# Kernel tuning notes

Measured on AMD Instinct MI355X. Metric: run time of the kernel, lower is better.

Reference implementation:

```python
import jax, jax.numpy as jnp
import numpy as np

B, H, F, E, K = 32, 4096, 4096, 8, 2

def setup_inputs() -> dict:
    key = jax.random.key(0)
    ks = jax.random.split(key, 5)
    x = jax.random.normal(ks[0], (B, H), dtype=jnp.float32)
    Wg = jax.random.normal(ks[1], (H, E), dtype=jnp.float32) * 0.02
    W1 = jax.random.normal(ks[2], (E, H, F), dtype=jnp.float32) * 0.02
    W3 = jax.random.normal(ks[3], (E, H, F), dtype=jnp.float32) * 0.02
    W2 = jax.random.normal(ks[4], (E, F, H), dtype=jnp.float32) * 0.02
    return {"x": x, "Wg": Wg, "W1": W1, "W3": W3, "W2": W2}

def reference(x, Wg, W1, W3, W2):
    # Gate: [B, E] logits, top-2 selection, softmax over the 2 selected logits
    logits = x @ Wg                                   # [B, E]
    vals, idx = jax.lax.top_k(logits, K)              # [B, K]
    w = jax.nn.softmax(vals, axis=-1)                 # [B, K]
    # Combine weights per expert: [B, E] (zero for unselected experts)
    combine = jnp.sum(jax.nn.one_hot(idx, E, dtype=x.dtype) * w[..., None], axis=1)
    h = jnp.einsum('bh,ehf->ebf', x, W1)              # [E, B, F]
    g = jax.nn.silu(h) * jnp.einsum('bh,ehf->ebf', x, W3)
    y = jnp.einsum('ebf,efh->ebh', g, W2)             # [E, B, H]
    # Scatter-combine: weighted sum over experts (all-gather + reduce-sum in source)
    return jnp.einsum('be,ebh->bh', combine, y)       # [B, H]
```

## Files before the change

kernel.cpp:

```cpp
#include <hip/hip_runtime.h>
#include <cstdint>

#define BB 32
#define HH 4096
#define FF 4096
#define EE 8
#define NSLOT 16
#define TSEG 16

__global__ __launch_bounds__(256) void gate_kernel(const float* __restrict__ x,
                                                   const float* __restrict__ Wg,
                                                   float* __restrict__ logits) {
  int b = blockIdx.x;
  int tid = threadIdx.x;
  float acc[EE];
#pragma unroll
  for (int e = 0; e < EE; ++e) acc[e] = 0.f;
  const float* xb = x + (size_t)b * HH;
  for (int h = tid; h < HH; h += 256) {
    float xv = xb[h];
    const float4* wg = (const float4*)(Wg + (size_t)h * EE);
    float4 w0 = wg[0], w1 = wg[1];
    acc[0] = fmaf(xv, w0.x, acc[0]);
    acc[1] = fmaf(xv, w0.y, acc[1]);
    acc[2] = fmaf(xv, w0.z, acc[2]);
    acc[3] = fmaf(xv, w0.w, acc[3]);
    acc[4] = fmaf(xv, w1.x, acc[4]);
    acc[5] = fmaf(xv, w1.y, acc[5]);
    acc[6] = fmaf(xv, w1.z, acc[6]);
    acc[7] = fmaf(xv, w1.w, acc[7]);
  }
#pragma unroll
  for (int off = 32; off > 0; off >>= 1) {
#pragma unroll
    for (int e = 0; e < EE; ++e) acc[e] += __shfl_down(acc[e], off, 64);
  }
  __shared__ float part[4][EE];
  if ((tid & 63) == 0) {
#pragma unroll
    for (int e = 0; e < EE; ++e) part[tid >> 6][e] = acc[e];
  }
  __syncthreads();
  if (tid < EE) {
    logits[(size_t)b * EE + tid] =
        part[0][tid] + part[1][tid] + part[2][tid] + part[3][tid];
  }
}

__global__ void route_kernel(const float* __restrict__ logits,
                             int* __restrict__ cnt,
                             int* __restrict__ tok,
                             float* __restrict__ wts) {
  if (threadIdx.x != 0 || blockIdx.x != 0) return;
  int e0[BB], e1[BB];
  float p0[BB], p1[BB];
  for (int b = 0; b < BB; ++b) {
    const float* L = logits + (size_t)b * EE;
    int i0 = 0;
    float v0 = L[0];
    for (int e = 1; e < EE; ++e) {
      float v = L[e];
      if (v > v0) { v0 = v; i0 = e; }
    }
    int i1 = (i0 == 0) ? 1 : 0;
    float v1 = L[i1];
    for (int e = 0; e < EE; ++e) {
      if (e == i0) continue;
      float v = L[e];
      if (v > v1) { v1 = v; i1 = e; }
    }
    float p = 1.f / (1.f + __expf(v1 - v0));
    e0[b] = i0; e1[b] = i1; p0[b] = p; p1[b] = 1.f - p;
  }
  for (int s = 0; s < NSLOT; ++s) {
    cnt[s] = 0;
    for (int t = 0; t < TSEG; ++t) { tok[s * TSEG + t] = 0; wts[s * TSEG + t] = 0.f; }
  }
  for (int e = 0; e < EE; ++e) {
    int c = 0;
    for (int b = 0; b < BB; ++b) {
      float w = 0.f;
      int sel = 0;
      if (e0[b] == e) { w = p0[b]; sel = 1; }
      else if (e1[b] == e) { w = p1[b]; sel = 1; }
      if (sel) {
        int s = e * 2 + (c >> 4);
        int t = c & 15;
        tok[s * TSEG + t] = b;
        wts[s * TSEG + t] = w;
        cnt[s] = t + 1;
        ++c;
      }
    }
  }
}

__global__ __launch_bounds__(256) void buildx_kernel(const float* __restrict__ x,
                                                     const int* __restrict__ cnt,
                                                     const int* __restrict__ tok,
                                                     float* __restrict__ xseg) {
  int s = blockIdx.y;
  int tid = threadIdx.x;
  int t = tid & 15;
  int hoff = tid >> 4;
  int c = cnt[s];
  int tk = tok[s * TSEG + t];
  bool act = t < c;
  int hbase = blockIdx.x * 256;
#pragma unroll
  for (int i = 0; i < 16; ++i) {
    int h = hbase + i * 16 + hoff;
    float v = act ? x[(size_t)tk * HH + h] : 0.f;
    xseg[((size_t)s * HH + h) * TSEG + t] = v;
  }
}

template <int NT>
__device__ __forceinline__ void fma_rowT(float4* __restrict__ acc,
                                         const float* __restrict__ xr, float4 wv) {
  float xs[NT];
#pragma unroll
  for (int q = 0; q < NT; q += 4) *(float4*)&xs[q] = *(const float4*)(xr + q);
#pragma unroll
  for (int t = 0; t < NT; ++t) {
    acc[t].x = fmaf(xs[t], wv.x, acc[t].x);
    acc[t].y = fmaf(xs[t], wv.y, acc[t].y);
    acc[t].z = fmaf(xs[t], wv.z, acc[t].z);
    acc[t].w = fmaf(xs[t], wv.w, acc[t].w);
  }
}

template <int NT>
__device__ __forceinline__ void accum_chunk256(float4* __restrict__ acc,
                                               const float* __restrict__ wp,
                                               const float* __restrict__ xr) {
  float4 ring[8];
#pragma unroll
  for (int k = 0; k < 8; ++k) ring[k] = *(const float4*)(wp + (size_t)k * 4096);
  for (int i0 = 0; i0 + 8 < 256; i0 += 8) {
#pragma unroll
    for (int k = 0; k < 8; ++k) {
      float4 wv = ring[k];
      ring[k] = *(const float4*)(wp + (size_t)(i0 + 8 + k) * 4096);
      fma_rowT<NT>(acc, xr + (size_t)(i0 + k) * NT, wv);
    }
  }
#pragma unroll
  for (int k = 0; k < 8; ++k)
    fma_rowT<NT>(acc, xr + (size_t)(248 + k) * NT, ring[k]);
}

template <int NT>
__device__ __forceinline__ void stageT(float* __restrict__ lx,
                                       const float* __restrict__ src, int tid) {
  const float4* s4 = (const float4*)src;
  float4* d4 = (float4*)lx;
#pragma unroll
  for (int k = 0; k < NT; ++k) {
    int q = k * 256 + tid;
    int row = q / (NT / 4);
    int part = q & ((NT / 4) - 1);
    d4[q] = s4[row * 4 + part];
  }
}

template <int NT>
__device__ __forceinline__ void reduce4(float* __restrict__ lx,
                                        const float4* __restrict__ acc,
                                        float* __restrict__ v, int tid) {
  int l = tid & 63;
  int w = tid >> 6;
  __syncthreads();
  float4* red = (float4*)lx;
#pragma unroll
  for (int t = 0; t < NT; ++t) red[(t * 4 + w) * 64 + l] = acc[t];
  __syncthreads();
  int lane = tid >> 2;
  int sub = tid & 3;
#pragma unroll
  for (int t = 0; t < NT; ++t) {
    float sum = 0.f;
#pragma unroll
    for (int w4 = 0; w4 < 4; ++w4)
      sum += lx[(((t * 4 + w4) * 64 + lane) << 2) + sub];
    v[t] = sum;
  }
}

template <int NT>
__device__ __forceinline__ void passB_body(const float* __restrict__ Wm,
                                           const float* __restrict__ xsrc,
                                           float* __restrict__ segbase,
                                           float* __restrict__ lx, int tid) {
  int l = tid & 63;
  int w = tid >> 6;
  float4 acc[NT];
#pragma unroll
  for (int t = 0; t < NT; ++t) acc[t] = make_float4(0.f, 0.f, 0.f, 0.f);
  for (int ch = 0; ch < 4; ++ch) {
    __syncthreads();
    stageT<NT>(lx, xsrc + (size_t)(ch * 1024) * TSEG, tid);
    __syncthreads();
    accum_chunk256<NT>(acc, Wm + (size_t)(ch * 1024 + w * 256) * FF + l * 4,
                       lx + (size_t)(w * 256) * NT);
  }
  float v[TSEG];
#pragma unroll
  for (int t = 0; t < TSEG; ++t) v[t] = 0.f;
  reduce4<NT>(lx, acc, v, tid);
  float* seg = segbase + (size_t)tid * TSEG;
#pragma unroll
  for (int q = 0; q < TSEG; q += 4) *(float4*)(seg + q) = *(const float4*)&v[q];
}

__global__ __launch_bounds__(256) void passB5_kernel(const float* __restrict__ W1,
                                                     const float* __restrict__ W3,
                                                     const float* __restrict__ xseg,
                                                     float* __restrict__ h1seg,
                                                     float* __restrict__ h3seg,
                                                     const int* __restrict__ cnt) {
  __shared__ float lx[1024 * TSEG];
  int s = blockIdx.y;
  int c = cnt[s];
  if (c == 0) return;
  int e = s >> 1;
  int mat = blockIdx.z;
  int colbase = blockIdx.x * 256;
  const float* Wm = (mat ? W3 : W1) + (size_t)e * HH * FF + colbase;
  const float* xsrc = xseg + (size_t)s * HH * TSEG;
  float* segbase = (mat ? h3seg : h1seg) + ((size_t)s * FF + colbase) * TSEG;
  if (c <= 8)
    passB_body<8>(Wm, xsrc, segbase, lx, threadIdx.x);
  else
    passB_body<16>(Wm, xsrc, segbase, lx, threadIdx.x);
}

__global__ __launch_bounds__(256) void silu_combine_kernel(float* __restrict__ h1seg,
                                                           const float* __restrict__ h3seg) {
  size_t i = (size_t)blockIdx.x * 256 + threadIdx.x;
  float4 h1 = ((const float4*)h1seg)[i];
  float4 h3 = ((const float4*)h3seg)[i];
  float4 r;
  r.x = (h1.x / (1.f + __expf(-h1.x))) * h3.x;
  r.y = (h1.y / (1.f + __expf(-h1.y))) * h3.y;
  r.z = (h1.z / (1.f + __expf(-h1.z))) * h3.z;
  r.w = (h1.w / (1.f + __expf(-h1.w))) * h3.w;
  ((float4*)h1seg)[i] = r;
}

template <int NT>
__device__ __forceinline__ void passC_body(const float* __restrict__ Wm,
                                           const float* __restrict__ gsrc,
                                           float* __restrict__ out,
                                           const int* __restrict__ stok,
                                           const float* __restrict__ swt,
                                           int c, int colbase,
                                           float* __restrict__ lx, int tid) {
  int l = tid & 63;
  int w = tid >> 6;
  float4 acc[NT];
#pragma unroll
  for (int t = 0; t < NT; ++t) acc[t] = make_float4(0.f, 0.f, 0.f, 0.f);
  for (int ch = 0; ch < 2; ++ch) {
    __syncthreads();
    stageT<NT>(lx, gsrc + (size_t)(ch * 1024) * TSEG, tid);
    __syncthreads();
    accum_chunk256<NT>(acc, Wm + (size_t)(ch * 1024 + w * 256) * HH + l * 4,
                       lx + (size_t)(w * 256) * NT);
  }
  float v[NT];
  reduce4<NT>(lx, acc, v, tid);
  float* op = out + colbase + tid;
#pragma unroll
  for (int t = 0; t < NT; ++t) {
    if (t < c) atomicAdd(op + (size_t)stok[t] * HH, swt[t] * v[t]);
  }
}

__global__ __launch_bounds__(256) void passC5_kernel(const float* __restrict__ W2,
                                                     const float* __restrict__ gseg,
                                                     const int* __restrict__ cnt,
                                                     const int* __restrict__ tok,
                                                     const float* __restrict__ wts,
                                                     float* __restrict__ out) {
  __shared__ float lx[1024 * TSEG];
  __shared__ int stok[TSEG];
  __shared__ float swt[TSEG];
  int s = blockIdx.y;
  int c = cnt[s];
  if (c == 0) return;
  int e = s >> 1;
  int z = blockIdx.z;
  int colbase = blockIdx.x * 256;
  if (threadIdx.x < TSEG) {
    stok[threadIdx.x] = tok[s * TSEG + threadIdx.x];
    swt[threadIdx.x] = wts[s * TSEG + threadIdx.x];
  }
  const float* Wm = W2 + (size_t)e * FF * HH + (size_t)(z * 2048) * HH + colbase;
  const float* gsrc = gseg + ((size_t)s * FF + z * 2048) * TSEG;
  if (c <= 8)
    passC_body<8>(Wm, gsrc, out, stok, swt, c, colbase, lx, threadIdx.x);
  else
    passC_body<16>(Wm, gsrc, out, stok, swt, c, colbase, lx, threadIdx.x);
}

extern "C" void kernel_launch(void* const* d_in, const int* in_sizes, int n_in,
                              void* d_out, int out_size, void* d_ws, size_t ws_size,
                              hipStream_t stream) {
  const float* x  = (const float*)d_in[0];
  const float* Wg = (const float*)d_in[1];
  const float* W1 = (const float*)d_in[2];
  const float* W3 = (const float*)d_in[3];
  const float* W2 = (const float*)d_in[4];
  float* out = (float*)d_out;

  char* ws = (char*)d_ws;
  float* logits = (float*)ws;
  int*   cnt    = (int*)(ws + 1024);
  int*   tok    = (int*)(ws + 1088);
  float* wts    = (float*)(ws + 2112);
  float* xseg   = (float*)(ws + 4096);
  float* h1seg  = xseg + (size_t)NSLOT * HH * TSEG;
  float* h3seg  = h1seg + (size_t)NSLOT * FF * TSEG;

  hipMemsetAsync(d_out, 0, (size_t)out_size * sizeof(float), stream);
  gate_kernel<<<BB, 256, 0, stream>>>(x, Wg, logits);
  route_kernel<<<1, 64, 0, stream>>>(logits, cnt, tok, wts);
  buildx_kernel<<<dim3(HH / 256, NSLOT), 256, 0, stream>>>(x, cnt, tok, xseg);
  passB5_kernel<<<dim3(FF / 256, NSLOT, 2), 256, 0, stream>>>(W1, W3, xseg, h1seg, h3seg, cnt);
  silu_combine_kernel<<<(NSLOT * FF * TSEG) / (256 * 4), 256, 0, stream>>>(h1seg, h3seg);
  passC5_kernel<<<dim3(HH / 256, NSLOT, 2), 256, 0, stream>>>(W2, h1seg, cnt, tok, wts, out);
}
```

Before: 419.3 us.

## Fuse SiLU into down-projection staging, narrow column tiles, order active slots first

Removes the separate SiLU-combine kernel by applying silu(h1)*h3 while staging activations into shared memory in the down-projection kernel. Each thread now handles float2 instead of float4 columns, so blocks cover 128 columns, doubling the grid and using a deeper 16-row weight prefetch ring. The routing kernel also emits an ordering that puts active slots first so early-exit blocks for empty slots are scheduled last, and buildx skips empty slots. This trades one kernel launch and a full intermediate round-trip for recomputing SiLU per column block, plus more blocks with narrower loads.

```diff
diff --git a/kernel.cpp b/kernel.cpp
--- a/kernel.cpp
+++ b/kernel.cpp
@@ -50,7 +50,8 @@
 __global__ void route_kernel(const float* __restrict__ logits,
                              int* __restrict__ cnt,
                              int* __restrict__ tok,
-                             float* __restrict__ wts) {
+                             float* __restrict__ wts,
+                             int* __restrict__ ord) {
   if (threadIdx.x != 0 || blockIdx.x != 0) return;
   int e0[BB], e1[BB];
   float p0[BB], p1[BB];
@@ -93,6 +94,9 @@
       }
     }
   }
+  int na = 0;
+  for (int s = 0; s < NSLOT; ++s) if (cnt[s] > 0) ord[na++] = s;
+  for (int s = 0; s < NSLOT; ++s) if (cnt[s] == 0) ord[na++] = s;
 }
 
 __global__ __launch_bounds__(256) void buildx_kernel(const float* __restrict__ x,
@@ -100,10 +104,11 @@
                                                      const int* __restrict__ tok,
                                                      float* __restrict__ xseg) {
   int s = blockIdx.y;
+  int c = cnt[s];
+  if (c == 0) return;
   int tid = threadIdx.x;
   int t = tid & 15;
   int hoff = tid >> 4;
-  int c = cnt[s];
   int tk = tok[s * TSEG + t];
   bool act = t < c;
   int hbase = blockIdx.x * 256;
@@ -116,8 +121,8 @@
 }
 
 template <int NT>
-__device__ __forceinline__ void fma_rowT(float4* __restrict__ acc,
-                                         const float* __restrict__ xr, float4 wv) {
+__device__ __forceinline__ void fma_row2(float2* __restrict__ acc,
+                                         const float* __restrict__ xr, float2 wv) {
   float xs[NT];
 #pragma unroll
   for (int q = 0; q < NT; q += 4) *(float4*)&xs[q] = *(const float4*)(xr + q);
@@ -125,29 +130,27 @@
   for (int t = 0; t < NT; ++t) {
     acc[t].x = fmaf(xs[t], wv.x, acc[t].x);
     acc[t].y = fmaf(xs[t], wv.y, acc[t].y);
-    acc[t].z = fmaf(xs[t], wv.z, acc[t].z);
-    acc[t].w = fmaf(xs[t], wv.w, acc[t].w);
-  }
-}
-
-template <int NT>
-__device__ __forceinline__ void accum_chunk256(float4* __restrict__ acc,
-                                               const float* __restrict__ wp,
-                                               const float* __restrict__ xr) {
-  float4 ring[8];
-#pragma unroll
-  for (int k = 0; k < 8; ++k) ring[k] = *(const float4*)(wp + (size_t)k * 4096);
-  for (int i0 = 0; i0 + 8 < 256; i0 += 8) {
-#pragma unroll
-    for (int k = 0; k < 8; ++k) {
-      float4 wv = ring[k];
-      ring[k] = *(const float4*)(wp + (size_t)(i0 + 8 + k) * 4096);
-      fma_rowT<NT>(acc, xr + (size_t)(i0 + k) * NT, wv);
-    }
-  }
-#pragma unroll
-  for (int k = 0; k < 8; ++k)
-    fma_rowT<NT>(acc, xr + (size_t)(248 + k) * NT, ring[k]);
+  }
+}
+
+template <int NT>
+__device__ __forceinline__ void accum256_f2(float2* __restrict__ acc,
+                                            const float* __restrict__ wp,
+                                            const float* __restrict__ xr) {
+  float2 ring[16];
+#pragma unroll
+  for (int k = 0; k < 16; ++k) ring[k] = *(const float2*)(wp + (size_t)k * 4096);
+  for (int i0 = 0; i0 + 16 < 256; i0 += 16) {
+#pragma unroll
+    for (int k = 0; k < 16; ++k) {
+      float2 wv = ring[k];
+      ring[k] = *(const float2*)(wp + (size_t)(i0 + 16 + k) * 4096);
+      fma_row2<NT>(acc, xr + (size_t)(i0 + k) * NT, wv);
+    }
+  }
+#pragma unroll
+  for (int k = 0; k < 16; ++k)
+    fma_row2<NT>(acc, xr + (size_t)(240 + k) * NT, ring[k]);
 }
 
 template <int NT>
@@ -165,25 +168,25 @@
 }
 
 template <int NT>
-__device__ __forceinline__ void reduce4(float* __restrict__ lx,
-                                        const float4* __restrict__ acc,
-                                        float* __restrict__ v, int tid) {
-  int l = tid & 63;
-  int w = tid >> 6;
-  __syncthreads();
-  float4* red = (float4*)lx;
-#pragma unroll
-  for (int t = 0; t < NT; ++t) red[(t * 4 + w) * 64 + l] = acc[t];
-  __syncthreads();
-  int lane = tid >> 2;
-  int sub = tid & 3;
-#pragma unroll
-  for (int t = 0; t < NT; ++t) {
-    float sum = 0.f;
-#pragma unroll
-    for (int w4 = 0; w4 < 4; ++w4)
-      sum += lx[(((t * 4 + w4) * 64 + lane) << 2) + sub];
-    v[t] = sum;
+__device__ __forceinline__ void stage_silu(float* __restrict__ lx,
+                                           const float* __restrict__ h1p,
+                                           const float* __restrict__ h3p, int tid) {
+  const float4* a4 = (const float4*)h1p;
+  const float4* b4 = (const float4*)h3p;
+  float4* d4 = (float4*)lx;
+#pragma unroll
+  for (int k = 0; k < NT; ++k) {
+    int q = k * 256 + tid;
+    int row = q / (NT / 4);
+    int part = q & ((NT / 4) - 1);
+    float4 a = a4[row * 4 + part];
+    float4 b = b4[row * 4 + part];
+    float4 g;
+    g.x = (a.x / (1.f + __expf(-a.x))) * b.x;
+    g.y = (a.y / (1.f + __expf(-a.y))) * b.y;
+    g.z = (a.z / (1.f + __expf(-a.z))) * b.z;
+    g.w = (a.w / (1.f + __expf(-a.w))) * b.w;
+    d4[q] = g;
   }
 }
 
@@ -194,38 +197,56 @@
                                            float* __restrict__ lx, int tid) {
   int l = tid & 63;
   int w = tid >> 6;
-  float4 acc[NT];
-#pragma unroll
-  for (int t = 0; t < NT; ++t) acc[t] = make_float4(0.f, 0.f, 0.f, 0.f);
+  float2 acc[NT];
+#pragma unroll
+  for (int t = 0; t < NT; ++t) acc[t] = make_float2(0.f, 0.f);
   for (int ch = 0; ch < 4; ++ch) {
     __syncthreads();
     stageT<NT>(lx, xsrc + (size_t)(ch * 1024) * TSEG, tid);
     __syncthreads();
-    accum_chunk256<NT>(acc, Wm + (size_t)(ch * 1024 + w * 256) * FF + l * 4,
-                       lx + (size_t)(w * 256) * NT);
-  }
-  float v[TSEG];
-#pragma unroll
-  for (int t = 0; t < TSEG; ++t) v[t] = 0.f;
-  reduce4<NT>(lx, acc, v, tid);
-  float* seg = segbase + (size_t)tid * TSEG;
-#pragma unroll
-  for (int q = 0; q < TSEG; q += 4) *(float4*)(seg + q) = *(const float4*)&v[q];
-}
-
-__global__ __launch_bounds__(256) void passB5_kernel(const float* __restrict__ W1,
+    accum256_f2<NT>(acc, Wm + (size_t)(ch * 1024 + w * 256) * FF + 2 * l,
+                    lx + (size_t)(w * 256) * NT);
+  }
+  __syncthreads();
+  float2* red = (float2*)lx;
+#pragma unroll
+  for (int t = 0; t < NT; ++t) red[(t * 4 + w) * 64 + l] = acc[t];
+  __syncthreads();
+  constexpr int TH = NT / 2;
+  int col_off = tid & 127;
+  int half = tid >> 7;
+  int lp = col_off >> 1;
+  int comp = col_off & 1;
+  float v[TH];
+#pragma unroll
+  for (int j = 0; j < TH; ++j) {
+    int t = half * TH + j;
+    float sum = 0.f;
+#pragma unroll
+    for (int w4 = 0; w4 < 4; ++w4)
+      sum += lx[(((t * 4 + w4) * 64 + lp) << 1) + comp];
+    v[j] = sum;
+  }
+  float* seg = segbase + (size_t)col_off * TSEG + half * TH;
+#pragma unroll
+  for (int q = 0; q < TH; q += 4) *(float4*)(seg + q) = *(const float4*)&v[q];
+}
+
+__global__ __launch_bounds__(256) void passB6_kernel(const float* __restrict__ W1,
                                                      const float* __restrict__ W3,
                                                      const float* __restrict__ xseg,
                                                      float* __restrict__ h1seg,
                                                      float* __restrict__ h3seg,
-                                                     const int* __restrict__ cnt) {
+                                                     const int* __restrict__ cnt,
+                                                     const int* __restrict__ ord) {
   __shared__ float lx[1024 * TSEG];
-  int s = blockIdx.y;
+  int gy = blockIdx.y;
+  int s = ord[gy >> 1];
+  int mat = gy & 1;
   int c = cnt[s];
   if (c == 0) return;
   int e = s >> 1;
-  int mat = blockIdx.z;
-  int colbase = blockIdx.x * 256;
+  int colbase = blockIdx.x * 128;
   const float* Wm = (mat ? W3 : W1) + (size_t)e * HH * FF + colbase;
   const float* xsrc = xseg + (size_t)s * HH * TSEG;
   float* segbase = (mat ? h3seg : h1seg) + ((size_t)s * FF + colbase) * TSEG;
@@ -235,22 +256,10 @@
     passB_body<16>(Wm, xsrc, segbase, lx, threadIdx.x);
 }
 
-__global__ __launch_bounds__(256) void silu_combine_kernel(float* __restrict__ h1seg,
-                                                           const float* __restrict__ h3seg) {
-  size_t i = (size_t)blockIdx.x * 256 + threadIdx.x;
-  float4 h1 = ((const float4*)h1seg)[i];
-  float4 h3 = ((const float4*)h3seg)[i];
-  float4 r;
-  r.x = (h1.x / (1.f + __expf(-h1.x))) * h3.x;
-  r.y = (h1.y / (1.f + __expf(-h1.y))) * h3.y;
-  r.z = (h1.z / (1.f + __expf(-h1.z))) * h3.z;
-  r.w = (h1.w / (1.f + __expf(-h1.w))) * h3.w;
-  ((float4*)h1seg)[i] = r;
-}
-
 template <int NT>
 __device__ __forceinline__ void passC_body(const float* __restrict__ Wm,
-                                           const float* __restrict__ gsrc,
+                                           const float* __restrict__ h1src,
+                                           const float* __restrict__ h3src,
                                            float* __restrict__ out,
                                            const int* __restrict__ stok,
                                            const float* __restrict__ swt,
@@ -258,50 +267,70 @@
                                            float* __restrict__ lx, int tid) {
   int l = tid & 63;
   int w = tid >> 6;
-  float4 acc[NT];
-#pragma unroll
-  for (int t = 0; t < NT; ++t) acc[t] = make_float4(0.f, 0.f, 0.f, 0.f);
+  float2 acc[NT];
+#pragma unroll
+  for (int t = 0; t < NT; ++t) acc[t] = make_float2(0.f, 0.f);
   for (int ch = 0; ch < 2; ++ch) {
     __syncthreads();
-    stageT<NT>(lx, gsrc + (size_t)(ch * 1024) * TSEG, tid);
+    stage_silu<NT>(lx, h1src + (size_t)(ch * 1024) * TSEG,
+                   h3src + (size_t)(ch * 1024) * TSEG, tid);
     __syncthreads();
-    accum_chunk256<NT>(acc, Wm + (size_t)(ch * 1024 + w * 256) * HH + l * 4,
-                       lx + (size_t)(w * 256) * NT);
-  }
-  float v[NT];
-  reduce4<NT>(lx, acc, v, tid);
-  float* op = out + colbase + tid;
-#pragma unroll
-  for (int t = 0; t < NT; ++t) {
-    if (t < c) atomicAdd(op + (size_t)stok[t] * HH, swt[t] * v[t]);
-  }
-}
-
-__global__ __launch_bounds__(256) void passC5_kernel(const float* __restrict__ W2,
-                                                     const float* __restrict__ gseg,
+    accum256_f2<NT>(acc, Wm + (size_t)(ch * 1024 + w * 256) * HH + 2 * l,
+                    lx + (size_t)(w * 256) * NT);
+  }
+  __syncthreads();
+  float2* red = (float2*)lx;
+#pragma unroll
+  for (int t = 0; t < NT; ++t) red[(t * 4 + w) * 64 + l] = acc[t];
+  __syncthreads();
+  constexpr int TH = NT / 2;
+  int col_off = tid & 127;
+  int half = tid >> 7;
+  int lp = col_off >> 1;
+  int comp = col_off & 1;
+  float* op = out + colbase + col_off;
+#pragma unroll
+  for (int j = 0; j < TH; ++j) {
+    int t = half * TH + j;
+    if (t < c) {
+      float sum = 0.f;
+#pragma unroll
+      for (int w4 = 0; w4 < 4; ++w4)
+        sum += lx[(((t * 4 + w4) * 64 + lp) << 1) + comp];
+      atomicAdd(op + (size_t)stok[t] * HH, swt[t] * sum);
+    }
+  }
+}
+
+__global__ __launch_bounds__(256) void passC6_kernel(const float* __restrict__ W2,
+                                                     const float* __restrict__ h1seg,
+                                                     const float* __restrict__ h3seg,
                                                      const int* __restrict__ cnt,
                                                      const int* __restrict__ tok,
                                                      const float* __restrict__ wts,
+                                                     const int* __restrict__ ord,
                                                      float* __restrict__ out) {
   __shared__ float lx[1024 * TSEG];
   __shared__ int stok[TSEG];
   __shared__ float swt[TSEG];
-  int s = blockIdx.y;
+  int gy = blockIdx.y;
+  int s = ord[gy >> 1];
+  int z = gy & 1;
   int c = cnt[s];
   if (c == 0) return;
   int e = s >> 1;
-  int z = blockIdx.z;
-  int colbase = blockIdx.x * 256;
+  int colbase = blockIdx.x * 128;
   if (threadIdx.x < TSEG) {
     stok[threadIdx.x] = tok[s * TSEG + threadIdx.x];
     swt[threadIdx.x] = wts[s * TSEG + threadIdx.x];
   }
   const float* Wm = W2 + (size_t)e * FF * HH + (size_t)(z * 2048) * HH + colbase;
-  const float* gsrc = gseg + ((size_t)s * FF + z * 2048) * TSEG;
+  const float* h1src = h1seg + ((size_t)s * FF + z * 2048) * TSEG;
+  const float* h3src = h3seg + ((size_t)s * FF + z * 2048) * TSEG;
   if (c <= 8)
-    passC_body<8>(Wm, gsrc, out, stok, swt, c, colbase, lx, threadIdx.x);
+    passC_body<8>(Wm, h1src, h3src, out, stok, swt, c, colbase, lx, threadIdx.x);
   else
-    passC_body<16>(Wm, gsrc, out, stok, swt, c, colbase, lx, threadIdx.x);
+    passC_body<16>(Wm, h1src, h3src, out, stok, swt, c, colbase, lx, threadIdx.x);
 }
 
 extern "C" void kernel_launch(void* const* d_in, const int* in_sizes, int n_in,
@@ -319,15 +348,15 @@
   int*   cnt    = (int*)(ws + 1024);
   int*   tok    = (int*)(ws + 1088);
   float* wts    = (float*)(ws + 2112);
+  int*   ord    = (int*)(ws + 3136);
   float* xseg   = (float*)(ws + 4096);
   float* h1seg  = xseg + (size_t)NSLOT * HH * TSEG;
   float* h3seg  = h1seg + (size_t)NSLOT * FF * TSEG;
 
   hipMemsetAsync(d_out, 0, (size_t)out_size * sizeof(float), stream);
   gate_kernel<<<BB, 256, 0, stream>>>(x, Wg, logits);
-  route_kernel<<<1, 64, 0, stream>>>(logits, cnt, tok, wts);
+  route_kernel<<<1, 64, 0, stream>>>(logits, cnt, tok, wts, ord);
   buildx_kernel<<<dim3(HH / 256, NSLOT), 256, 0, stream>>>(x, cnt, tok, xseg);
-  passB5_kernel<<<dim3(FF / 256, NSLOT, 2), 256, 0, stream>>>(W1, W3, xseg, h1seg, h3seg, cnt);
-  silu_combine_kernel<<<(NSLOT * FF * TSEG) / (256 * 4), 256, 0, stream>>>(h1seg, h3seg);
-  passC5_kernel<<<dim3(HH / 256, NSLOT, 2), 256, 0, stream>>>(W2, h1seg, cnt, tok, wts, out);
-}
+  passB6_kernel<<<dim3(FF / 128, NSLOT * 2), 256, 0, stream>>>(W1, W3, xseg, h1seg, h3seg, cnt, ord);
+  passC6_kernel<<<dim3(HH / 128, NSLOT * 2), 256, 0, stream>>>(W2, h1seg, h3seg, cnt, tok, wts, ord, out);
+}
```

Result: faster. 403.2 us (-3.9%).
